# Kernel tuning notes

Measured on AMD Instinct MI355X. Metric: run time of the kernel, lower is better.

## Reference

```python
import jax, jax.numpy as jnp
import numpy as np

B, C, NS, NP = 8, 128, 32, 128  # batch, channels, nsample, npoint


def setup_inputs() -> dict:
    key = jax.random.key(0)
    k1, k2 = jax.random.split(key)
    points = jax.random.normal(k1, (B, C, NS, NP), dtype=jnp.float32)
    gamma = jax.random.uniform(k2, (1,), dtype=jnp.float32)
    return {"points": points, "gamma": gamma}


def reference(points, gamma):
    b, c, ns, npnt = points.shape
    x = points.reshape(b, c, ns * npnt)              # [B, C, N]
    # energy[b, n, m] = sum_c x[b,c,n] * x[b,c,m]   (QK^T with Q=K=x^T)
    energy = jnp.einsum('bcn,bcm->bnm', x, x)
    # max-subtraction variant: softmax(max_row - energy)
    energy_new = jnp.max(energy, axis=-1, keepdims=True) - energy
    attention = jax.nn.softmax(energy_new, axis=-1)   # [B, N, N]
    # points_attention = V @ attention^T : out[b,c,n] = sum_m x[b,c,m]*attn[b,n,m]
    out = jnp.einsum('bcm,bnm->bcn', x, attention)
    out = out.reshape(b, c, ns, npnt)
    return gamma * out + points
```

## Files before the change

kernel.cpp:

```cpp
#include <hip/hip_runtime.h>
#include <stdint.h>

#define NB_ 8
#define NC_ 128
#define NN_ 4096

typedef float f32x4 __attribute__((ext_vector_type(4)));
typedef _Float16 f16x8 __attribute__((ext_vector_type(8)));
typedef short s16x8 __attribute__((ext_vector_type(8)));
typedef unsigned short u16x4 __attribute__((ext_vector_type(4)));

__device__ __forceinline__ uint16_t f2bf(float f) {
    union { float f; uint32_t u; } v; v.f = f;
    return (uint16_t)((v.u + 0x7FFFu + ((v.u >> 16) & 1u)) >> 16);
}
__device__ __forceinline__ uint16_t f2bf_trunc(float f) {
    union { float f; uint32_t u; } v; v.f = f;
    return (uint16_t)(v.u >> 16);
}
__device__ __forceinline__ float bf2f(uint16_t b) {
    union { uint32_t u; float f; } v; v.u = ((uint32_t)b) << 16;
    return v.f;
}

__global__ __launch_bounds__(256) void prep_kernel(
        const float* __restrict__ pts, _Float16* __restrict__ xt,
        _Float16* __restrict__ Kf, uint16_t* __restrict__ Vf) {
    __shared__ float T[64][65];
    int bid = blockIdx.x;
    int ct = bid & 1, nt = (bid >> 1) & 63, b = bid >> 7;
    int c0 = ct * 64, n0 = nt * 64;
    int lr = threadIdx.x >> 6, lc = threadIdx.x & 63;
    const float* src = pts + ((size_t)b * NC_ + c0) * NN_ + n0;
#pragma unroll
    for (int r = 0; r < 16; ++r) {
        int cl = r * 4 + lr;
        T[cl][lc] = src[(size_t)cl * NN_ + lc];
    }
    __syncthreads();
#pragma unroll
    for (int r = 0; r < 16; ++r) {
        int nl = r * 4 + lr;
        xt[((size_t)b * NN_ + n0 + nl) * NC_ + c0 + lc] = (_Float16)T[lc][nl];
    }

    int w = threadIdx.x >> 6, l = threadIdx.x & 63, l15 = l & 15, g = l >> 4;
    _Float16* Kfb = Kf + (size_t)b * 524288;
    uint16_t* Vfb = Vf + (size_t)b * 524288;
#pragma unroll
    for (int e = 0; e < 2; ++e) {
        int q2 = w + e * 4;
        int tl = q2 >> 2, msq = (q2 >> 1) & 1, ccl = q2 & 1;
        int t = nt * 2 + tl, cc = ct * 2 + ccl;
        f16x8 kv;
#pragma unroll
        for (int j = 0; j < 8; ++j)
            kv[j] = (_Float16)T[ccl * 32 + g * 8 + j][tl * 32 + msq * 16 + l15];
        *(f16x8*)(Kfb + (((size_t)t * 8 + msq * 4 + cc) * 64 + l) * 8) = kv;
    }
#pragma unroll
    for (int e = 0; e < 2; ++e) {
        int q2 = w + e * 4;
        int tl = q2 >> 2, csl = q2 & 3;
        int t = nt * 2 + tl, cs = ct * 4 + csl;
        s16x8 vv;
#pragma unroll
        for (int j = 0; j < 8; ++j)
            vv[j] = (short)f2bf(T[csl * 16 + l15][tl * 32 + g * 8 + j]);
        *(s16x8*)(Vfb + (((size_t)t * 8 + cs) * 64 + l) * 8) = vv;
    }
}

template <int MSPLIT>
__global__ __launch_bounds__(256, 2) void flash_kernel(
        const _Float16* __restrict__ xt, const _Float16* __restrict__ Kf,
        const uint16_t* __restrict__ Vf,
        uint16_t* __restrict__ Opart, float* __restrict__ lpart,
        const float* __restrict__ pts, const float* __restrict__ gamma,
        float* __restrict__ out) {
    int bid = blockIdx.x;
    int b = bid & 7;
    int rest = bid >> 3;
    int nb = rest & 15;
    int mh = rest >> 4;
    int tid = threadIdx.x;
    int w = tid >> 6, l = tid & 63, l15 = l & 15, g = l >> 4;

    __shared__ __align__(16) uint16_t Kt[2 * 4096];
    __shared__ __align__(16) uint16_t Vt[2 * 4096];
    __shared__ __align__(16) uint16_t Plds[4][64][40];
    __shared__ float Lsh[4][64];

    int nbase = nb * 256 + w * 64;
    const _Float16* xtb = xt + (size_t)b * NN_ * NC_;
    const char* KfB = (const char*)(Kf + (size_t)b * 524288);
    const char* VfB = (const char*)(Vf + (size_t)b * 524288);
    char* KtB = (char*)Kt;
    char* VtB = (char*)Vt;
    int so = tid * 16;

#define STAGE(TILE, BUF) do {                                                          \
        size_t gb_ = (size_t)(TILE) * 8192 + so;                                       \
        int lb_ = (BUF) * 8192 + so;                                                   \
        __builtin_amdgcn_global_load_lds(                                              \
            (const __attribute__((address_space(1))) void*)(KfB + gb_),                \
            (__attribute__((address_space(3))) void*)(KtB + lb_), 16, 0, 0);           \
        __builtin_amdgcn_global_load_lds(                                              \
            (const __attribute__((address_space(1))) void*)(KfB + gb_ + 4096),         \
            (__attribute__((address_space(3))) void*)(KtB + lb_ + 4096), 16, 0, 0);    \
        __builtin_amdgcn_global_load_lds(                                              \
            (const __attribute__((address_space(1))) void*)(VfB + gb_),                \
            (__attribute__((address_space(3))) void*)(VtB + lb_), 16, 0, 0);           \
        __builtin_amdgcn_global_load_lds(                                              \
            (const __attribute__((address_space(1))) void*)(VfB + gb_ + 4096),         \
            (__attribute__((address_space(3))) void*)(VtB + lb_ + 4096), 16, 0, 0);    \
    } while (0)

    f16x8 q[4][4];
#pragma unroll
    for (int ns = 0; ns < 4; ++ns)
#pragma unroll
        for (int cc = 0; cc < 4; ++cc)
            q[ns][cc] = *(const f16x8*)(xtb + (size_t)(nbase + ns * 16 + l15) * NC_ + cc * 32 + g * 8);

    f32x4 acc[8][4];
#pragma unroll
    for (int cs = 0; cs < 8; ++cs)
#pragma unroll
        for (int ns = 0; ns < 4; ++ns)
            acc[cs][ns] = (f32x4){0.f, 0.f, 0.f, 0.f};
    float lsum[4][4];
#pragma unroll
    for (int ns = 0; ns < 4; ++ns)
#pragma unroll
        for (int r = 0; r < 4; ++r) lsum[ns][r] = 0.f;

    const int nsteps = (MSPLIT == 4) ? 32 : 128;
    const int tile0 = mh * nsteps;

    STAGE(tile0, 0);

    for (int it = 0; it < nsteps; ++it) {
        __syncthreads();
        int cur = it & 1, nxt = cur ^ 1;
        if (it + 1 < nsteps) STAGE(tile0 + it + 1, nxt);

        const _Float16* Kc = (const _Float16*)(Kt + cur * 4096);
        const uint16_t* Vc = Vt + cur * 4096;

#pragma unroll
        for (int ms = 0; ms < 2; ++ms) {
            f16x8 kf[4];
#pragma unroll
            for (int cc = 0; cc < 4; ++cc)
                kf[cc] = *(const f16x8*)(Kc + (ms * 4 + cc) * 512 + l * 8);
#pragma unroll
            for (int h = 0; h < 2; ++h) {
                f32x4 sa = (f32x4){0.f, 0.f, 0.f, 0.f};
                f32x4 sb = (f32x4){0.f, 0.f, 0.f, 0.f};
                __builtin_amdgcn_s_setprio(1);
#pragma unroll
                for (int cc = 0; cc < 4; ++cc) {
                    sa = __builtin_amdgcn_mfma_f32_16x16x32_f16(q[2 * h][cc], kf[cc], sa, 0, 0, 0);
                    sb = __builtin_amdgcn_mfma_f32_16x16x32_f16(q[2 * h + 1][cc], kf[cc], sb, 0, 0, 0);
                }
                __builtin_amdgcn_s_setprio(0);
#pragma unroll
                for (int r = 0; r < 4; ++r) {
                    float p0 = __expf(-(sa[r] + 64.f));
                    float p1 = __expf(-(sb[r] + 64.f));
                    lsum[2 * h][r] += p0;
                    lsum[2 * h + 1][r] += p1;
                    Plds[w][(2 * h) * 16 + g * 4 + r][ms * 16 + l15] = f2bf_trunc(p0);
                    Plds[w][(2 * h + 1) * 16 + g * 4 + r][ms * 16 + l15] = f2bf_trunc(p1);
                }
            }
        }
        asm volatile("s_waitcnt lgkmcnt(0)" ::: "memory");

        s16x8 pf[4];
#pragma unroll
        for (int ns = 0; ns < 4; ++ns)
            pf[ns] = *(const s16x8*)&Plds[w][ns * 16 + l15][g * 8];

        __builtin_amdgcn_s_setprio(1);
#pragma unroll
        for (int cs = 0; cs < 8; ++cs) {
            s16x8 vf = *(const s16x8*)(Vc + cs * 512 + l * 8);
#pragma unroll
            for (int ns = 0; ns < 4; ++ns)
                acc[cs][ns] = __builtin_amdgcn_mfma_f32_16x16x32_bf16(vf, pf[ns], acc[cs][ns], 0, 0, 0);
        }
        __builtin_amdgcn_s_setprio(0);
    }
#undef STAGE

#pragma unroll
    for (int ns = 0; ns < 4; ++ns)
#pragma unroll
        for (int r = 0; r < 4; ++r) {
            float v2 = lsum[ns][r];
            v2 += __shfl_xor(v2, 1, 16);
            v2 += __shfl_xor(v2, 2, 16);
            v2 += __shfl_xor(v2, 4, 16);
            v2 += __shfl_xor(v2, 8, 16);
            lsum[ns][r] = v2;
        }

    if (l15 == 0) {
#pragma unroll
        for (int ns = 0; ns < 4; ++ns)
#pragma unroll
            for (int r = 0; r < 4; ++r)
                Lsh[w][ns * 16 + g * 4 + r] = lsum[ns][r];
    }
    asm volatile("s_waitcnt lgkmcnt(0)" ::: "memory");
    __syncthreads();
    float linv[4];
#pragma unroll
    for (int ns = 0; ns < 4; ++ns) linv[ns] = 1.0f / Lsh[w][ns * 16 + l15];

    if (MSPLIT > 1) {
        uint16_t* opb = Opart + (size_t)((b * 16 + nb) * MSPLIT + mh) * 32768;
#pragma unroll
        for (int cs = 0; cs < 8; ++cs)
#pragma unroll
            for (int ns = 0; ns < 4; ++ns)
#pragma unroll
                for (int r = 0; r < 4; ++r)
                    opb[(cs * 16 + g * 4 + r) * 256 + w * 64 + ns * 16 + l15] =
                        f2bf(acc[cs][ns][r] * linv[ns]);
        if (l15 == 0) {
            size_t lb = (size_t)((b * 16 + nb) * MSPLIT + mh) * 256;
#pragma unroll
            for (int ns = 0; ns < 4; ++ns)
#pragma unroll
                for (int r = 0; r < 4; ++r)
                    lpart[lb + w * 64 + ns * 16 + g * 4 + r] = lsum[ns][r];
        }
    } else {
        float gm = gamma[0];
        const float* ptsb = pts + (size_t)b * NC_ * NN_;
        float* outb = out + (size_t)b * NC_ * NN_;
#pragma unroll
        for (int cs = 0; cs < 8; ++cs)
#pragma unroll
            for (int ns = 0; ns < 4; ++ns)
#pragma unroll
                for (int r = 0; r < 4; ++r) {
                    size_t idx = (size_t)(cs * 16 + g * 4 + r) * NN_ + nbase + ns * 16 + l15;
                    outb[idx] = gm * acc[cs][ns][r] * linv[ns] + ptsb[idx];
                }
    }
}

template <int NS>
__global__ __launch_bounds__(256) void epi_kernel(
        const float* __restrict__ pts, const float* __restrict__ gamma,
        const uint16_t* __restrict__ Opart, const float* __restrict__ lpart,
        float* __restrict__ out) {
    size_t t = (size_t)blockIdx.x * 256 + threadIdx.x;
    size_t e = t * 4;
    int b = (int)(e >> 19);
    int r = (int)(e & 524287);
    int c = r >> 12;
    int n = r & 4095;
    int nb = n >> 8, nl = n & 255;
    int base = (b * 16 + nb) * NS;
    f32x4 osum = (f32x4){0.f, 0.f, 0.f, 0.f};
    f32x4 lsum = (f32x4){0.f, 0.f, 0.f, 0.f};
#pragma unroll
    for (int i = 0; i < NS; ++i) {
        u16x4 o16 = *(const u16x4*)(Opart + (size_t)(base + i) * 32768 + c * 256 + nl);
        f32x4 li = *(const f32x4*)(lpart + (size_t)(base + i) * 256 + nl);
#pragma unroll
        for (int j = 0; j < 4; ++j) {
            osum[j] += bf2f(o16[j]) * li[j];
            lsum[j] += li[j];
        }
    }
    f32x4 p = *(const f32x4*)(pts + e);
    float gm = gamma[0];
    f32x4 res;
#pragma unroll
    for (int j = 0; j < 4; ++j)
        res[j] = gm * osum[j] / lsum[j] + p[j];
    *(f32x4*)(out + e) = res;
}

extern "C" void kernel_launch(void* const* d_in, const int* in_sizes, int n_in,
                              void* d_out, int out_size, void* d_ws, size_t ws_size,
                              hipStream_t stream) {
    const float* pts = (const float*)d_in[0];
    const float* gamma = (const float*)d_in[1];
    float* out = (float*)d_out;

    char* ws = (char*)d_ws;
    _Float16* xt = (_Float16*)ws;
    _Float16* Kf = (_Float16*)(ws + 8388608);
    uint16_t* Vf = (uint16_t*)(ws + 16777216);
    uint16_t* Opart = (uint16_t*)(ws + 25165824);
    float* lpart = (float*)(ws + 25165824 + 33554432);
    const size_t WS4 = 25165824ull + 33554432ull + 524288ull;

    prep_kernel<<<1024, 256, 0, stream>>>(pts, xt, Kf, Vf);
    if (ws_size >= WS4) {
        flash_kernel<4><<<512, 256, 0, stream>>>(xt, Kf, Vf, Opart, lpart, pts, gamma, out);
        epi_kernel<4><<<4096, 256, 0, stream>>>(pts, gamma, Opart, lpart, out);
    } else {
        flash_kernel<1><<<128, 256, 0, stream>>>(xt, Kf, Vf, nullptr, nullptr, pts, gamma, out);
    }
}
```

Before: 99.72 us.

## Keep softmax probabilities in registers by computing transposed scores and using 16x16x16 bf16 MFMA

Swaps the MFMA operand order so each lane's score accumulator already matches the B-operand layout of a 16x16x16 bf16 MFMA. The exponentiated probabilities can then feed the PV product straight from registers, with no round trip through the Plds shared-memory buffer and no lgkmcnt wait. V is re-laid out in the prep kernel into 4-element fragments, and the row-sum reduction becomes a two-step cross-group shuffle with no shared memory or barrier. The cost is twice as many smaller MFMA instructions for the PV product, plus changed register and LDS use per block.

```diff
diff --git a/kernel.cpp b/kernel.cpp
--- a/kernel.cpp
+++ b/kernel.cpp
@@ -8,6 +8,7 @@
 typedef float f32x4 __attribute__((ext_vector_type(4)));
 typedef _Float16 f16x8 __attribute__((ext_vector_type(8)));
 typedef short s16x8 __attribute__((ext_vector_type(8)));
+typedef short s16x4 __attribute__((ext_vector_type(4)));
 typedef unsigned short u16x4 __attribute__((ext_vector_type(4)));
 
 __device__ __forceinline__ uint16_t f2bf(float f) {
@@ -63,11 +64,14 @@
         int q2 = w + e * 4;
         int tl = q2 >> 2, csl = q2 & 3;
         int t = nt * 2 + tl, cs = ct * 4 + csl;
-        s16x8 vv;
-#pragma unroll
-        for (int j = 0; j < 8; ++j)
-            vv[j] = (short)f2bf(T[csl * 16 + l15][tl * 32 + g * 8 + j]);
-        *(s16x8*)(Vfb + (((size_t)t * 8 + cs) * 64 + l) * 8) = vv;
+#pragma unroll
+        for (int ms = 0; ms < 2; ++ms) {
+            u16x4 vv;
+#pragma unroll
+            for (int j = 0; j < 4; ++j)
+                vv[j] = f2bf(T[csl * 16 + l15][tl * 32 + ms * 16 + g * 4 + j]);
+            *(u16x4*)(Vfb + ((size_t)(t * 16 + ms * 8 + cs) * 64 + l) * 4) = vv;
+        }
     }
 }
 
@@ -88,8 +92,6 @@
 
     __shared__ __align__(16) uint16_t Kt[2 * 4096];
     __shared__ __align__(16) uint16_t Vt[2 * 4096];
-    __shared__ __align__(16) uint16_t Plds[4][64][40];
-    __shared__ float Lsh[4][64];
 
     int nbase = nb * 256 + w * 64;
     const _Float16* xtb = xt + (size_t)b * NN_ * NC_;
@@ -129,11 +131,7 @@
 #pragma unroll
         for (int ns = 0; ns < 4; ++ns)
             acc[cs][ns] = (f32x4){0.f, 0.f, 0.f, 0.f};
-    float lsum[4][4];
-#pragma unroll
-    for (int ns = 0; ns < 4; ++ns)
-#pragma unroll
-        for (int r = 0; r < 4; ++r) lsum[ns][r] = 0.f;
+    float lsum[4] = {0.f, 0.f, 0.f, 0.f};
 
     const int nsteps = (MSPLIT == 4) ? 32 : 128;
     const int tile0 = mh * nsteps;
@@ -154,71 +152,52 @@
 #pragma unroll
             for (int cc = 0; cc < 4; ++cc)
                 kf[cc] = *(const f16x8*)(Kc + (ms * 4 + cc) * 512 + l * 8);
-#pragma unroll
-            for (int h = 0; h < 2; ++h) {
-                f32x4 sa = (f32x4){0.f, 0.f, 0.f, 0.f};
-                f32x4 sb = (f32x4){0.f, 0.f, 0.f, 0.f};
+
+            s16x4 pf[4];
+#pragma unroll
+            for (int ns = 0; ns < 4; ++ns) {
+                f32x4 s = (f32x4){0.f, 0.f, 0.f, 0.f};
                 __builtin_amdgcn_s_setprio(1);
 #pragma unroll
-                for (int cc = 0; cc < 4; ++cc) {
-                    sa = __builtin_amdgcn_mfma_f32_16x16x32_f16(q[2 * h][cc], kf[cc], sa, 0, 0, 0);
-                    sb = __builtin_amdgcn_mfma_f32_16x16x32_f16(q[2 * h + 1][cc], kf[cc], sb, 0, 0, 0);
-                }
+                for (int cc = 0; cc < 4; ++cc)
+                    s = __builtin_amdgcn_mfma_f32_16x16x32_f16(kf[cc], q[ns][cc], s, 0, 0, 0);
                 __builtin_amdgcn_s_setprio(0);
-#pragma unroll
-                for (int r = 0; r < 4; ++r) {
-                    float p0 = __expf(-(sa[r] + 64.f));
-                    float p1 = __expf(-(sb[r] + 64.f));
-                    lsum[2 * h][r] += p0;
-                    lsum[2 * h + 1][r] += p1;
-                    Plds[w][(2 * h) * 16 + g * 4 + r][ms * 16 + l15] = f2bf_trunc(p0);
-                    Plds[w][(2 * h + 1) * 16 + g * 4 + r][ms * 16 + l15] = f2bf_trunc(p1);
-                }
+                float p0 = __expf(-(s[0] + 64.f));
+                float p1 = __expf(-(s[1] + 64.f));
+                float p2 = __expf(-(s[2] + 64.f));
+                float p3 = __expf(-(s[3] + 64.f));
+                lsum[ns] += (p0 + p1) + (p2 + p3);
+                s16x4 t;
+                t[0] = (short)f2bf_trunc(p0);
+                t[1] = (short)f2bf_trunc(p1);
+                t[2] = (short)f2bf_trunc(p2);
+                t[3] = (short)f2bf_trunc(p3);
+                pf[ns] = t;
             }
-        }
-        asm volatile("s_waitcnt lgkmcnt(0)" ::: "memory");
-
-        s16x8 pf[4];
-#pragma unroll
-        for (int ns = 0; ns < 4; ++ns)
-            pf[ns] = *(const s16x8*)&Plds[w][ns * 16 + l15][g * 8];
-
-        __builtin_amdgcn_s_setprio(1);
-#pragma unroll
-        for (int cs = 0; cs < 8; ++cs) {
-            s16x8 vf = *(const s16x8*)(Vc + cs * 512 + l * 8);
-#pragma unroll
-            for (int ns = 0; ns < 4; ++ns)
-                acc[cs][ns] = __builtin_amdgcn_mfma_f32_16x16x32_bf16(vf, pf[ns], acc[cs][ns], 0, 0, 0);
-        }
-        __builtin_amdgcn_s_setprio(0);
+
+            __builtin_amdgcn_s_setprio(1);
+#pragma unroll
+            for (int cs = 0; cs < 8; ++cs) {
+                s16x4 vf = *(const s16x4*)(Vc + (ms * 8 + cs) * 256 + l * 4);
+#pragma unroll
+                for (int ns = 0; ns < 4; ++ns)
+                    acc[cs][ns] = __builtin_amdgcn_mfma_f32_16x16x16bf16_1k(
+                        vf, pf[ns], acc[cs][ns], 0, 0, 0);
+            }
+            __builtin_amdgcn_s_setprio(0);
+        }
     }
 #undef STAGE
 
-#pragma unroll
-    for (int ns = 0; ns < 4; ++ns)
-#pragma unroll
-        for (int r = 0; r < 4; ++r) {
-            float v2 = lsum[ns][r];
-            v2 += __shfl_xor(v2, 1, 16);
-            v2 += __shfl_xor(v2, 2, 16);
-            v2 += __shfl_xor(v2, 4, 16);
-            v2 += __shfl_xor(v2, 8, 16);
-            lsum[ns][r] = v2;
-        }
-
-    if (l15 == 0) {
-#pragma unroll
-        for (int ns = 0; ns < 4; ++ns)
-#pragma unroll
-            for (int r = 0; r < 4; ++r)
-                Lsh[w][ns * 16 + g * 4 + r] = lsum[ns][r];
-    }
-    asm volatile("s_waitcnt lgkmcnt(0)" ::: "memory");
-    __syncthreads();
-    float linv[4];
-#pragma unroll
-    for (int ns = 0; ns < 4; ++ns) linv[ns] = 1.0f / Lsh[w][ns * 16 + l15];
+    float lred[4], linv[4];
+#pragma unroll
+    for (int ns = 0; ns < 4; ++ns) {
+        float v2 = lsum[ns];
+        v2 += __shfl_xor(v2, 16);
+        v2 += __shfl_xor(v2, 32);
+        lred[ns] = v2;
+        linv[ns] = 1.0f / v2;
+    }
 
     if (MSPLIT > 1) {
         uint16_t* opb = Opart + (size_t)((b * 16 + nb) * MSPLIT + mh) * 32768;
@@ -230,13 +209,11 @@
                 for (int r = 0; r < 4; ++r)
                     opb[(cs * 16 + g * 4 + r) * 256 + w * 64 + ns * 16 + l15] =
                         f2bf(acc[cs][ns][r] * linv[ns]);
-        if (l15 == 0) {
+        if (g == 0) {
             size_t lb = (size_t)((b * 16 + nb) * MSPLIT + mh) * 256;
 #pragma unroll
             for (int ns = 0; ns < 4; ++ns)
-#pragma unroll
-                for (int r = 0; r < 4; ++r)
-                    lpart[lb + w * 64 + ns * 16 + g * 4 + r] = lsum[ns][r];
+                lpart[lb + w * 64 + ns * 16 + l15] = lred[ns];
         }
     } else {
         float gm = gamma[0];
```

Result: slower. 103.8 us (+4.1%).
